# Kernel tuning notes

Measured on AMD Instinct MI355X. Metric: run time of the kernel, lower is better.

The kernel has to match this reference:

```python
import jax, jax.numpy as jnp
import numpy as np

W1 = 1.0
W2 = 1.0


def setup_inputs() -> dict:
    key = jax.random.key(0)
    k1, k2 = jax.random.split(key)
    points1 = jax.random.normal(k1, (8, 4096, 3), dtype=jnp.float32)
    points2 = jax.random.normal(k2, (8, 4096, 3), dtype=jnp.float32)
    return {"points1": points1, "points2": points2}


def reference(points1, points2):
    # Pairwise squared L2 distances: [B, N1, N2].
    # (torch code does sqrt(dist)**2 which is mathematically identity for dist>=0.)
    diff = points1[:, :, None, :] - points2[:, None, :, :]  # [B, N1, N2, 3]
    dist = jnp.sum(diff * diff, axis=3)                      # [B, N1, N2]
    dist_min1 = jnp.min(dist, axis=2)  # nearest in points2 for each points1: [B, N1]
    dist_min2 = jnp.min(dist, axis=1)  # nearest in points1 for each points2: [B, N2]
    loss1 = dist_min1.mean(axis=1)     # [B]
    loss2 = dist_min2.mean(axis=1)     # [B]
    loss = W1 * loss1 + W2 * loss2
    return loss.mean()  # each_batch=False
```

## Files before the change

kernel.cpp:

```cpp
#include <hip/hip_runtime.h>
#include <float.h>


#define NBATCH 8
#define NPTS   4096
#define NCHUNK 16
#define CHUNK  (NPTS / NCHUNK)
#define BLK    256
#define PTS    4
#define ATILE  (BLK * PTS)
#define NATILE (NPTS / ATILE)

__global__ __launch_bounds__(BLK)
void chamfer_min_kernel(const float* __restrict__ p1,
                        const float* __restrict__ p2,
                        unsigned int* __restrict__ mins )
{
    __shared__ float4 sB[CHUNK];

    int bid   = blockIdx.x;
    int chunk = bid & (NCHUNK - 1);  bid >>= 4;
    int atile = bid & (NATILE - 1);  bid >>= 2;
    int b     = bid & (NBATCH - 1);  bid >>= 3;
    int dir   = bid;

    const float* A    = dir ? p2 : p1;
    const float* Bpts = dir ? p1 : p2;
    int tid = threadIdx.x;

    {
        int j = chunk * CHUNK + tid;
        const float* src = Bpts + ((size_t)b * NPTS + j) * 3;
        float x = src[0], y = src[1], z = src[2];
        sB[tid] = make_float4(x, y, z, x * x + y * y + z * z);
    }
    __syncthreads();

    float m2x[PTS], m2y[PTS], m2z[PTS], n1[PTS], best[PTS];
    int abase = atile * ATILE;
#pragma unroll
    for (int k = 0; k < PTS; ++k) {
        int ai = abase + tid + k * BLK;
        const float* src = A + ((size_t)b * NPTS + ai) * 3;
        float x = src[0], y = src[1], z = src[2];
        m2x[k] = -2.0f * x;
        m2y[k] = -2.0f * y;
        m2z[k] = -2.0f * z;
        n1[k]  = x * x + y * y + z * z;
        best[k] = FLT_MAX;
    }

#pragma unroll 4
    for (int j = 0; j < CHUNK; ++j) {
        float4 q = sB[j];
#pragma unroll
        for (int k = 0; k < PTS; ++k) {
            float t = fmaf(m2x[k], q.x, q.w);
            t = fmaf(m2y[k], q.y, t);
            t = fmaf(m2z[k], q.z, t);
            best[k] = fminf(best[k], t);
        }
    }

    unsigned int* marr = mins + ((size_t)dir * NBATCH + b) * NPTS + abase + tid;
#pragma unroll
    for (int k = 0; k < PTS; ++k) {
        float d = fmaxf(best[k] + n1[k], 0.0f);
        atomicMin(&marr[k * BLK], __float_as_uint(d));
    }
}

__global__ __launch_bounds__(1024)
void chamfer_reduce_kernel(const float* __restrict__ mins, float* __restrict__ out)
{
    __shared__ float wave_sums[16];
    float s = 0.0f;
    for (int i = threadIdx.x; i < 2 * NBATCH * NPTS; i += 1024)
        s += mins[i];
#pragma unroll
    for (int off = 32; off > 0; off >>= 1)
        s += __shfl_down(s, off, 64);
    int wave = threadIdx.x >> 6;
    if ((threadIdx.x & 63) == 0) wave_sums[wave] = s;
    __syncthreads();
    if (threadIdx.x < 16) {
        s = wave_sums[threadIdx.x];
#pragma unroll
        for (int off = 8; off > 0; off >>= 1)
            s += __shfl_down(s, off, 16);
        if (threadIdx.x == 0) out[0] = s / (float)(NBATCH * NPTS);
    }
}

extern "C" void kernel_launch(void* const* d_in, const int* in_sizes, int n_in,
                              void* d_out, int out_size, void* d_ws, size_t ws_size,
                              hipStream_t stream) {
    const float* p1 = (const float*)d_in[0];
    const float* p2 = (const float*)d_in[1];
    float* out = (float*)d_out;
    unsigned int* mins = (unsigned int*)d_ws;

    hipMemsetAsync(d_ws, 0xFF, (size_t)2 * NBATCH * NPTS * sizeof(unsigned int), stream);

    int nblocks = 2 * NBATCH * NATILE * NCHUNK;
    chamfer_min_kernel<<<nblocks, BLK, 0, stream>>>(p1, p2, mins);
    chamfer_reduce_kernel<<<1, 1024, 0, stream>>>((const float*)d_ws, out);
}
```

Measured before the change: 93.97 us.

## Use packed FP32 FMA with SoA shared tiles and larger per-thread point tiles

Restructures the min kernel so each thread handles 16 query points covering the whole point set, while blocks split the other set into 32 chunks of 128. Reference points are stored in shared memory as pairs laid out so two candidates can be processed together with 2-wide vector FMAs, which can map to packed FP32 instructions on CDNA. The final reduction kernel is also vectorised to float4 loads. The aim is to double FMA throughput and raise arithmetic per shared load. The cost is a grid of only 512 blocks, which lowers occupancy, and higher register pressure.

```diff
diff --git a/kernel.cpp b/kernel.cpp
--- a/kernel.cpp
+++ b/kernel.cpp
@@ -2,25 +2,26 @@
 #include <float.h>
 
 
+typedef float v2f __attribute__((ext_vector_type(2)));
+
 #define NBATCH 8
 #define NPTS   4096
-#define NCHUNK 16
+#define BLK    256
+#define PTS    16
+#define NCHUNK 32
 #define CHUNK  (NPTS / NCHUNK)
-#define BLK    256
-#define PTS    4
-#define ATILE  (BLK * PTS)
-#define NATILE (NPTS / ATILE)
+#define PAIRS  (CHUNK / 2)
 
 __global__ __launch_bounds__(BLK)
 void chamfer_min_kernel(const float* __restrict__ p1,
                         const float* __restrict__ p2,
                         unsigned int* __restrict__ mins )
 {
-    __shared__ float4 sB[CHUNK];
+    __shared__ float4 sXY[PAIRS];
+    __shared__ float4 sZW[PAIRS];
 
     int bid   = blockIdx.x;
-    int chunk = bid & (NCHUNK - 1);  bid >>= 4;
-    int atile = bid & (NATILE - 1);  bid >>= 2;
+    int chunk = bid & (NCHUNK - 1);  bid >>= 5;
     int b     = bid & (NBATCH - 1);  bid >>= 3;
     int dir   = bid;
 
@@ -28,44 +29,54 @@
     const float* Bpts = dir ? p1 : p2;
     int tid = threadIdx.x;
 
-    {
-        int j = chunk * CHUNK + tid;
-        const float* src = Bpts + ((size_t)b * NPTS + j) * 3;
-        float x = src[0], y = src[1], z = src[2];
-        sB[tid] = make_float4(x, y, z, x * x + y * y + z * z);
+    if (tid < PAIRS) {
+        const float* s = Bpts + ((size_t)b * NPTS + chunk * CHUNK + 2 * tid) * 3;
+        float x0 = s[0], y0 = s[1], z0 = s[2];
+        float x1 = s[3], y1 = s[4], z1 = s[5];
+        sXY[tid] = make_float4(x0, x1, y0, y1);
+        sZW[tid] = make_float4(z0, z1,
+                               x0 * x0 + y0 * y0 + z0 * z0,
+                               x1 * x1 + y1 * y1 + z1 * z1);
+    }
+
+    v2f  m2x[PTS], m2y[PTS], m2z[PTS];
+    float n1[PTS], bestE[PTS], bestO[PTS];
+#pragma unroll
+    for (int k = 0; k < PTS; ++k) {
+        const float* s = A + ((size_t)b * NPTS + tid + k * BLK) * 3;
+        float x = s[0], y = s[1], z = s[2];
+        float mx = -2.0f * x, my = -2.0f * y, mz = -2.0f * z;
+        m2x[k] = (v2f){mx, mx};
+        m2y[k] = (v2f){my, my};
+        m2z[k] = (v2f){mz, mz};
+        n1[k]  = x * x + y * y + z * z;
+        bestE[k] = FLT_MAX;
+        bestO[k] = FLT_MAX;
     }
     __syncthreads();
 
-    float m2x[PTS], m2y[PTS], m2z[PTS], n1[PTS], best[PTS];
-    int abase = atile * ATILE;
-#pragma unroll
-    for (int k = 0; k < PTS; ++k) {
-        int ai = abase + tid + k * BLK;
-        const float* src = A + ((size_t)b * NPTS + ai) * 3;
-        float x = src[0], y = src[1], z = src[2];
-        m2x[k] = -2.0f * x;
-        m2y[k] = -2.0f * y;
-        m2z[k] = -2.0f * z;
-        n1[k]  = x * x + y * y + z * z;
-        best[k] = FLT_MAX;
-    }
-
-#pragma unroll 4
-    for (int j = 0; j < CHUNK; ++j) {
-        float4 q = sB[j];
+#pragma unroll 2
+    for (int p = 0; p < PAIRS; ++p) {
+        float4 xy = sXY[p];
+        float4 zw = sZW[p];
+        v2f qx = (v2f){xy.x, xy.y};
+        v2f qy = (v2f){xy.z, xy.w};
+        v2f qz = (v2f){zw.x, zw.y};
+        v2f qw = (v2f){zw.z, zw.w};
 #pragma unroll
         for (int k = 0; k < PTS; ++k) {
-            float t = fmaf(m2x[k], q.x, q.w);
-            t = fmaf(m2y[k], q.y, t);
-            t = fmaf(m2z[k], q.z, t);
-            best[k] = fminf(best[k], t);
+            v2f t = __builtin_elementwise_fma(m2x[k], qx, qw);
+            t = __builtin_elementwise_fma(m2y[k], qy, t);
+            t = __builtin_elementwise_fma(m2z[k], qz, t);
+            bestE[k] = fminf(bestE[k], t.x);
+            bestO[k] = fminf(bestO[k], t.y);
         }
     }
 
-    unsigned int* marr = mins + ((size_t)dir * NBATCH + b) * NPTS + abase + tid;
+    unsigned int* marr = mins + ((size_t)dir * NBATCH + b) * NPTS + tid;
 #pragma unroll
     for (int k = 0; k < PTS; ++k) {
-        float d = fmaxf(best[k] + n1[k], 0.0f);
+        float d = fmaxf(fminf(bestE[k], bestO[k]) + n1[k], 0.0f);
         atomicMin(&marr[k * BLK], __float_as_uint(d));
     }
 }
@@ -74,9 +85,13 @@
 void chamfer_reduce_kernel(const float* __restrict__ mins, float* __restrict__ out)
 {
     __shared__ float wave_sums[16];
+    const float4* m4 = (const float4*)mins;
     float s = 0.0f;
-    for (int i = threadIdx.x; i < 2 * NBATCH * NPTS; i += 1024)
-        s += mins[i];
+#pragma unroll
+    for (int i = 0; i < 16; ++i) {
+        float4 v = m4[threadIdx.x + i * 1024];
+        s += (v.x + v.y) + (v.z + v.w);
+    }
 #pragma unroll
     for (int off = 32; off > 0; off >>= 1)
         s += __shfl_down(s, off, 64);
@@ -102,7 +117,7 @@
 
     hipMemsetAsync(d_ws, 0xFF, (size_t)2 * NBATCH * NPTS * sizeof(unsigned int), stream);
 
-    int nblocks = 2 * NBATCH * NATILE * NCHUNK;
+    int nblocks = 2 * NBATCH * NCHUNK;
     chamfer_min_kernel<<<nblocks, BLK, 0, stream>>>(p1, p2, mins);
     chamfer_reduce_kernel<<<1, 1024, 0, stream>>>((const float*)d_ws, out);
 }
```

Measured after the change: 81.09 us. 13.7% less time.
